# Optimization experiments

Hardware: AMD Instinct MI355X
Metric: run time of the kernel (lower is better)

## Reference

```python
import jax, jax.numpy as jnp
import numpy as np

B, LATENT = 8192, 1024
NR, NC = 12, 12                      # nb_rows, nb_cols
H0, W0 = NR + 2, NC + 2              # 14x14 after reshape
EPS = 1e-5
SLOPE = 0.01                         # LeakyReLU default


def setup_inputs() -> dict:
    key = jax.random.key(0)
    ks = jax.random.split(key, 9)
    s = 0.05
    return {
        "x": jax.random.normal(ks[0], (B, LATENT), jnp.float32),
        "fc_w": jax.random.normal(ks[1], (H0 * W0 * 36, LATENT), jnp.float32) * s,
        "fc_b": jax.random.normal(ks[2], (H0 * W0 * 36,), jnp.float32) * s,
        "conv_w": jax.random.normal(ks[3], (16, 36, 2, 2), jnp.float32) * s,
        "conv_b": jax.random.normal(ks[4], (16,), jnp.float32) * s,
        "gamma": jnp.ones((16,), jnp.float32),
        "beta": jnp.zeros((16,), jnp.float32),
        # locally-connected weights: (out_ch, in_ch, Hout, Wout, k*k)
        "lw1": jax.random.normal(ks[5], (6, 16, H0 - 1, W0 - 1, 4), jnp.float32) * s,
        "lw2": jax.random.normal(ks[6], (1, 6, H0 - 2, W0 - 2, 4), jnp.float32) * s,
    }


def _leaky(x):
    return jnp.where(x >= 0, x, SLOPE * x)


def _local_conv2(x, w):
    # x: (B,C,H,W); w: (O,C,Ho,Wo,4) with k=2, stride 1, no padding
    Ho, Wo = w.shape[2], w.shape[3]
    patches = jnp.stack(
        [x[:, :, dy:dy + Ho, dx:dx + Wo] for dy in (0, 1) for dx in (0, 1)],
        axis=-1)  # (B,C,Ho,Wo,4)
    return jnp.einsum('bchwk,ochwk->bohw', patches, w)


def reference(x, fc_w, fc_b, conv_w, conv_b, gamma, beta, lw1, lw2):
    # fc -> view(B, H0, W0, 36) -> permute to NCHW
    h = x @ fc_w.T + fc_b
    h = h.reshape(B, H0, W0, 36).transpose(0, 3, 1, 2)  # (B,36,14,14)
    # Conv2d k=2 padding='same' (torch pads bottom/right for even kernels)
    h = jax.lax.conv_general_dilated(
        h, conv_w, window_strides=(1, 1), padding=((0, 1), (0, 1)),
        dimension_numbers=('NCHW', 'OIHW', 'NCHW')) + conv_b[None, :, None, None]
    h = _leaky(h)
    # BatchNorm2d (training mode: batch stats, biased var)
    mu = h.mean(axis=(0, 2, 3), keepdims=True)
    var = h.var(axis=(0, 2, 3), keepdims=True)
    h = (h - mu) * jax.lax.rsqrt(var + EPS)
    h = h * gamma[None, :, None, None] + beta[None, :, None, None]
    # locally-connected stack: 14x14 -> 13x13 -> 12x12
    h = _leaky(_local_conv2(h, lw1))
    return _local_conv2(h, lw2)  # (B,1,12,12)
```

## Files before the change

### kernel.cpp

```cpp
#include <hip/hip_runtime.h>


#define SLOPE 0.01f

typedef __bf16 bf16x8 __attribute__((ext_vector_type(8)));
typedef float f32x4 __attribute__((ext_vector_type(4)));

typedef const __attribute__((address_space(1))) void* gas_ptr;
typedef __attribute__((address_space(3))) void* las_ptr;

__device__ __forceinline__ void load16_to_lds(const void* g, void* l) {
  __builtin_amdgcn_global_load_lds((gas_ptr)g, (las_ptr)l, 16, 0, 0);
}

__device__ __forceinline__ unsigned short f2bf(float f) {
  union { float f; unsigned int u; } v; v.f = f;
  unsigned int r = v.u + 0x7FFFu + ((v.u >> 16) & 1u);
  return (unsigned short)(r >> 16);
}
__device__ __forceinline__ float bfbits2f(unsigned int bits16) {
  union { unsigned int u; float f; } v; v.u = bits16 << 16;
  return v.f;
}
__device__ __forceinline__ float leaky(float v) { return v >= 0.f ? v : SLOPE * v; }

__global__ void k_cast_x(const float* __restrict__ x, unsigned short* __restrict__ xb,
                         float* __restrict__ stats_col) {
  if (blockIdx.x == 0)
    for (int i = threadIdx.x; i < 6400; i += 256) stats_col[i] = 0.f;
  int gid = blockIdx.x * 256 + threadIdx.x;
  const float4* x4 = (const float4*)x;
  float4 a = x4[gid * 2], b = x4[gid * 2 + 1];
  union { unsigned short s[8]; uint4 v; } o;
  o.s[0] = f2bf(a.x); o.s[1] = f2bf(a.y); o.s[2] = f2bf(a.z); o.s[3] = f2bf(a.w);
  o.s[4] = f2bf(b.x); o.s[5] = f2bf(b.y); o.s[6] = f2bf(b.z); o.s[7] = f2bf(b.w);
  ((uint4*)xb)[gid] = o.v;
}

__global__ void k_fold(const float* __restrict__ fc_w, const float* __restrict__ fc_b,
                       const float* __restrict__ conv_w, const float* __restrict__ conv_b,
                       unsigned short* __restrict__ Wc, float* __restrict__ bc) {
  int blk = blockIdx.y, kq = blockIdx.x, t = threadIdx.x;
  if (blk == 196) {
    uint4 z = make_uint4(0, 0, 0, 0);
    for (int i = t; i < 64 * 64; i += 256) {
      int r = i >> 6, qq = i & 63;
      *(uint4*)(Wc + (3136 + r) * 1024 + kq * 256 + qq * 8) = z;
    }
    if (kq == 0) for (int i = 3136 + t; i < 3200; i += 256) bc[i] = 0.f;
    return;
  }
  __shared__ float cw[2304];
  for (int i = t; i < 2304; i += 256) cw[i] = conv_w[i];
  __syncthreads();
  int i0 = blk / 14, j0 = blk - (blk / 14) * 14;
  int k = kq * 256 + t;
  float acc[16];
#pragma unroll
  for (int o = 0; o < 16; o++) acc[o] = 0.f;
  for (int c = 0; c < 36; c++) {
#pragma unroll
    for (int dy = 0; dy < 2; dy++) {
      int ii = i0 + dy; if (ii > 13) continue;
#pragma unroll
      for (int dx = 0; dx < 2; dx++) {
        int jj = j0 + dx; if (jj > 13) continue;
        float f = fc_w[((ii * 14 + jj) * 36 + c) * 1024 + k];
        int kk = dy * 2 + dx;
#pragma unroll
        for (int o = 0; o < 16; o++) acc[o] += cw[(o * 36 + c) * 4 + kk] * f;
      }
    }
  }
#pragma unroll
  for (int o = 0; o < 16; o++)
    Wc[(o * 196 + i0 * 14 + j0) * 1024 + k] = f2bf(acc[o]);
  if (kq == 0 && t < 16) {
    int o = t;
    float b = conv_b[o];
    for (int c = 0; c < 36; c++)
      for (int dy = 0; dy < 2; dy++) {
        int ii = i0 + dy; if (ii > 13) continue;
        for (int dx = 0; dx < 2; dx++) {
          int jj = j0 + dx; if (jj > 13) continue;
          b += cw[(o * 36 + c) * 4 + dy * 2 + dx] * fc_b[(ii * 14 + jj) * 36 + c];
        }
      }
    bc[o * 196 + i0 * 14 + j0] = b;
  }
}

__global__ __launch_bounds__(256, 2) void k_gemm(const unsigned short* __restrict__ Xb,
                                                 const unsigned short* __restrict__ Wcb,
                                                 const float* __restrict__ bc,
                                                 unsigned short* __restrict__ h2,
                                                 float* __restrict__ stats_col) {
  __shared__ __align__(16) char lds[16384];
  const int t = threadIdx.x;
  const int w = t >> 6, lane = t & 63;
  const int quad = lane >> 4, l15 = lane & 15;
  const int lid = blockIdx.x;
  const int m0 = (lid & 63) * 128, n0 = (lid >> 6) * 128;
  const int mrow = t & 127, tko = t >> 7;
  const unsigned short* ga = Xb + (m0 + mrow) * 1024 + tko * 8;
  const unsigned short* gb = Wcb + (n0 + mrow) * 1024 + tko * 8;
  char* lA = lds;
  char* lB = lds + 8192;
  const int wbase = w * 1024;
  const int wm0 = (w >> 1) * 64, wn0 = (w & 1) * 64;

  f32x4 acc[4][4];
#pragma unroll
  for (int a = 0; a < 4; a++)
#pragma unroll
    for (int b = 0; b < 4; b++) acc[a][b] = (f32x4){0.f, 0.f, 0.f, 0.f};

  for (int kb = 0; kb < 1024; kb += 32) {
    __syncthreads();
    load16_to_lds(ga + kb,      lA + wbase);
    load16_to_lds(ga + kb + 16, lA + 4096 + wbase);
    load16_to_lds(gb + kb,      lB + wbase);
    load16_to_lds(gb + kb + 16, lB + 4096 + wbase);
    __syncthreads();

    bf16x8 af[4], bfr[4];
#pragma unroll
    for (int mb = 0; mb < 4; mb++)
      af[mb] = *(const bf16x8*)(lA + quad * 2048 + (wm0 + mb * 16 + l15) * 16);
#pragma unroll
    for (int nb = 0; nb < 4; nb++)
      bfr[nb] = *(const bf16x8*)(lB + quad * 2048 + (wn0 + nb * 16 + l15) * 16);
#pragma unroll
    for (int mb = 0; mb < 4; mb++)
#pragma unroll
      for (int nb = 0; nb < 4; nb++)
        acc[mb][nb] = __builtin_amdgcn_mfma_f32_16x16x32_bf16(af[mb], bfr[nb], acc[mb][nb], 0, 0, 0);
  }

#pragma unroll
  for (int nb = 0; nb < 4; nb++) {
    int col = n0 + wn0 + nb * 16 + l15;
    float bias = bc[col];
    float s = 0.f, s2 = 0.f;
    unsigned short* base = h2 + col * 8192 + m0 + wm0 + quad * 4;
#pragma unroll
    for (int mb = 0; mb < 4; mb++) {
      union { unsigned short u[4]; uint2 v; } pk;
#pragma unroll
      for (int r = 0; r < 4; r++) {
        float v = leaky(acc[mb][nb][r] + bias);
        s += v; s2 += v * v;
        pk.u[r] = f2bf(v);
      }
      *(uint2*)(base + mb * 16) = pk.v;
    }
    s  += __shfl_xor(s, 16, 64);  s  += __shfl_xor(s, 32, 64);
    s2 += __shfl_xor(s2, 16, 64); s2 += __shfl_xor(s2, 32, 64);
    if (quad == 0) {
      atomicAdd(&stats_col[col], s);
      atomicAdd(&stats_col[3200 + col], s2);
    }
  }
}

__global__ void k_bnscale(const float* __restrict__ stats_col,
                          const float* __restrict__ gamma, const float* __restrict__ beta,
                          float* __restrict__ scbuf) {
  __shared__ float chs[16], chs2[16];
  int t = threadIdx.x;
  if (t < 16) { chs[t] = 0.f; chs2[t] = 0.f; }
  __syncthreads();
  for (int col = t; col < 3136; col += 256) {
    int o = col / 196;
    atomicAdd(&chs[o], stats_col[col]);
    atomicAdd(&chs2[o], stats_col[3200 + col]);
  }
  __syncthreads();
  if (t < 16) {
    const float inv = 1.f / 1605632.f;
    float mean = chs[t] * inv;
    float var = chs2[t] * inv - mean * mean;
    float sc = gamma[t] * rsqrtf(var + 1e-5f);
    scbuf[t] = sc; scbuf[16 + t] = beta[t] - mean * sc;
  }
}

__global__ __launch_bounds__(64) void k_tail1(const unsigned short* __restrict__ h2,
                                              const float* __restrict__ scbuf,
                                              const float* __restrict__ lw1,
                                              unsigned short* __restrict__ h4) {
  const int m = blockIdx.x * 64 + threadIdx.x;
  const int y = blockIdx.y;
  float acc[6][13];
#pragma unroll
  for (int o = 0; o < 6; o++)
#pragma unroll
    for (int x = 0; x < 13; x++) acc[o][x] = 0.f;

  for (int c = 0; c < 16; c++) {
    float scc = scbuf[c], shc = scbuf[16 + c];
    const unsigned short* p0 = h2 + (c * 196 + y * 14) * 8192 + m;
    float r0[14], r1[14];
#pragma unroll
    for (int x = 0; x < 14; x++) {
      r0[x] = bfbits2f(p0[x * 8192]) * scc + shc;
      r1[x] = bfbits2f(p0[(14 + x) * 8192]) * scc + shc;
    }
#pragma unroll
    for (int o = 0; o < 6; o++) {
      const float* wp = lw1 + (((o * 16 + c) * 13 + y) * 13) * 4;
#pragma unroll
      for (int x = 0; x < 13; x++)
        acc[o][x] += r0[x] * wp[4 * x] + r0[x + 1] * wp[4 * x + 1] +
                     r1[x] * wp[4 * x + 2] + r1[x + 1] * wp[4 * x + 3];
    }
  }
  unsigned short* q = h4 + y * 13 * 8192 + m;
#pragma unroll
  for (int o = 0; o < 6; o++)
#pragma unroll
    for (int x = 0; x < 13; x++)
      q[(o * 169 + x) * 8192] = f2bf(leaky(acc[o][x]));
}

__global__ __launch_bounds__(256) void k_tail2(const unsigned short* __restrict__ h4,
                                               const float* __restrict__ lw2,
                                               float* __restrict__ out) {
  const int lane = threadIdx.x & 63, w = threadIdx.x >> 6;
  const int m = blockIdx.x * 64 + lane;
  const int y = blockIdx.y * 4 + w;
  float acc[12];
#pragma unroll
  for (int x = 0; x < 12; x++) acc[x] = 0.f;
  for (int c = 0; c < 6; c++) {
    const unsigned short* p = h4 + (c * 13 + y) * 13 * 8192 + m;
    float r0[13], r1[13];
#pragma unroll
    for (int x = 0; x < 13; x++) {
      r0[x] = bfbits2f(p[x * 8192]);
      r1[x] = bfbits2f(p[(13 + x) * 8192]);
    }
    const float* wp = lw2 + ((c * 12 + y) * 12) * 4;
#pragma unroll
    for (int x = 0; x < 12; x++)
      acc[x] += r0[x] * wp[4 * x] + r0[x + 1] * wp[4 * x + 1] +
                r1[x] * wp[4 * x + 2] + r1[x + 1] * wp[4 * x + 3];
  }
  float* op = out + m * 144 + y * 12;
#pragma unroll
  for (int x = 0; x < 12; x++) op[x] = acc[x];
}

extern "C" void kernel_launch(void* const* d_in, const int* in_sizes, int n_in,
                              void* d_out, int out_size, void* d_ws, size_t ws_size,
                              hipStream_t stream) {
  const float* x      = (const float*)d_in[0];
  const float* fc_w   = (const float*)d_in[1];
  const float* fc_b   = (const float*)d_in[2];
  const float* conv_w = (const float*)d_in[3];
  const float* conv_b = (const float*)d_in[4];
  const float* gamma  = (const float*)d_in[5];
  const float* beta   = (const float*)d_in[6];
  const float* lw1    = (const float*)d_in[7];
  const float* lw2    = (const float*)d_in[8];

  char* ws = (char*)d_ws;
  unsigned short* Xb        = (unsigned short*)(ws);
  unsigned short* h4T       = (unsigned short*)(ws);
  unsigned short* Wc        = (unsigned short*)(ws + 16777216);
  float*          bc        = (float*)(ws + 23330816);
  float*          stats_col = (float*)(ws + 23343616);
  float*          scbuf     = (float*)(ws + 23369216);
  unsigned short* h2T       = (unsigned short*)(ws + 23369344);

  k_cast_x<<<4096, 256, 0, stream>>>(x, Xb, stats_col);
  k_fold<<<dim3(4, 197), 256, 0, stream>>>(fc_w, fc_b, conv_w, conv_b, Wc, bc);
  k_gemm<<<1600, 256, 0, stream>>>(Xb, Wc, bc, h2T, stats_col);
  k_bnscale<<<1, 256, 0, stream>>>(stats_col, gamma, beta, scbuf);
  k_tail1<<<dim3(128, 13), 64, 0, stream>>>(h2T, scbuf, lw1, h4T);
  k_tail2<<<dim3(128, 3), 256, 0, stream>>>(h4T, lw2, (float*)d_out);
}
```

Measured before the change: 444.3 us.

## Double-buffer GEMM with register prefetch and fuse prep and BN-scale kernels

The GEMM now stages global loads through registers into two LDS buffers. The next K-tile's loads are issued before the MFMAs and the tile is stored to the other buffer afterwards, so each iteration needs one barrier instead of two and memory latency can overlap with compute. Occupancy is raised to three blocks per SM. The x-cast and weight-fold kernels are merged into a single launch, and the BN scale/shift reduction is folded into the first tail kernel, which now uses 256-thread blocks. This removes two launches, but every tail block repeats the small per-channel stat reduction. The prefetch also reads slightly past row ends on the last iterations.

```diff
diff --git a/kernel.cpp b/kernel.cpp
--- a/kernel.cpp
+++ b/kernel.cpp
@@ -5,13 +5,6 @@
 
 typedef __bf16 bf16x8 __attribute__((ext_vector_type(8)));
 typedef float f32x4 __attribute__((ext_vector_type(4)));
-
-typedef const __attribute__((address_space(1))) void* gas_ptr;
-typedef __attribute__((address_space(3))) void* las_ptr;
-
-__device__ __forceinline__ void load16_to_lds(const void* g, void* l) {
-  __builtin_amdgcn_global_load_lds((gas_ptr)g, (las_ptr)l, 16, 0, 0);
-}
 
 __device__ __forceinline__ unsigned short f2bf(float f) {
   union { float f; unsigned int u; } v; v.f = f;
@@ -24,27 +17,30 @@
 }
 __device__ __forceinline__ float leaky(float v) { return v >= 0.f ? v : SLOPE * v; }
 
-__global__ void k_cast_x(const float* __restrict__ x, unsigned short* __restrict__ xb,
-                         float* __restrict__ stats_col) {
-  if (blockIdx.x == 0)
-    for (int i = threadIdx.x; i < 6400; i += 256) stats_col[i] = 0.f;
-  int gid = blockIdx.x * 256 + threadIdx.x;
-  const float4* x4 = (const float4*)x;
-  float4 a = x4[gid * 2], b = x4[gid * 2 + 1];
-  union { unsigned short s[8]; uint4 v; } o;
-  o.s[0] = f2bf(a.x); o.s[1] = f2bf(a.y); o.s[2] = f2bf(a.z); o.s[3] = f2bf(a.w);
-  o.s[4] = f2bf(b.x); o.s[5] = f2bf(b.y); o.s[6] = f2bf(b.z); o.s[7] = f2bf(b.w);
-  ((uint4*)xb)[gid] = o.v;
-}
-
-__global__ void k_fold(const float* __restrict__ fc_w, const float* __restrict__ fc_b,
+__global__ void k_prep(const float* __restrict__ x, unsigned short* __restrict__ xb,
+                       float* __restrict__ stats_col,
+                       const float* __restrict__ fc_w, const float* __restrict__ fc_b,
                        const float* __restrict__ conv_w, const float* __restrict__ conv_b,
                        unsigned short* __restrict__ Wc, float* __restrict__ bc) {
-  int blk = blockIdx.y, kq = blockIdx.x, t = threadIdx.x;
+  const int t = threadIdx.x;
+  if (blockIdx.x < 4096) {
+    if (blockIdx.x == 0)
+      for (int i = t; i < 6400; i += 256) stats_col[i] = 0.f;
+    int gid = blockIdx.x * 256 + t;
+    const float4* x4 = (const float4*)x;
+    float4 a = x4[gid * 2], b = x4[gid * 2 + 1];
+    union { unsigned short s[8]; uint4 v; } o;
+    o.s[0] = f2bf(a.x); o.s[1] = f2bf(a.y); o.s[2] = f2bf(a.z); o.s[3] = f2bf(a.w);
+    o.s[4] = f2bf(b.x); o.s[5] = f2bf(b.y); o.s[6] = f2bf(b.z); o.s[7] = f2bf(b.w);
+    ((uint4*)xb)[gid] = o.v;
+    return;
+  }
+  int bid = blockIdx.x - 4096;
+  int kq = bid & 3, blk = bid >> 2;
   if (blk == 196) {
     uint4 z = make_uint4(0, 0, 0, 0);
-    for (int i = t; i < 64 * 64; i += 256) {
-      int r = i >> 6, qq = i & 63;
+    for (int i = t; i < 64 * 32; i += 256) {
+      int r = i >> 5, qq = i & 31;
       *(uint4*)(Wc + (3136 + r) * 1024 + kq * 256 + qq * 8) = z;
     }
     if (kq == 0) for (int i = 3136 + t; i < 3200; i += 256) bc[i] = 0.f;
@@ -90,12 +86,12 @@
   }
 }
 
-__global__ __launch_bounds__(256, 2) void k_gemm(const unsigned short* __restrict__ Xb,
+__global__ __launch_bounds__(256, 3) void k_gemm(const unsigned short* __restrict__ Xb,
                                                  const unsigned short* __restrict__ Wcb,
                                                  const float* __restrict__ bc,
                                                  unsigned short* __restrict__ h2,
                                                  float* __restrict__ stats_col) {
-  __shared__ __align__(16) char lds[16384];
+  __shared__ __align__(16) char lds[32768];
   const int t = threadIdx.x;
   const int w = t >> 6, lane = t & 63;
   const int quad = lane >> 4, l15 = lane & 15;
@@ -104,9 +100,7 @@
   const int mrow = t & 127, tko = t >> 7;
   const unsigned short* ga = Xb + (m0 + mrow) * 1024 + tko * 8;
   const unsigned short* gb = Wcb + (n0 + mrow) * 1024 + tko * 8;
-  char* lA = lds;
-  char* lB = lds + 8192;
-  const int wbase = w * 1024;
+  char* const wA = lds + tko * 2048 + mrow * 16;
   const int wm0 = (w >> 1) * 64, wn0 = (w & 1) * 64;
 
   f32x4 acc[4][4];
@@ -115,26 +109,42 @@
 #pragma unroll
     for (int b = 0; b < 4; b++) acc[a][b] = (f32x4){0.f, 0.f, 0.f, 0.f};
 
-  for (int kb = 0; kb < 1024; kb += 32) {
-    __syncthreads();
-    load16_to_lds(ga + kb,      lA + wbase);
-    load16_to_lds(ga + kb + 16, lA + 4096 + wbase);
-    load16_to_lds(gb + kb,      lB + wbase);
-    load16_to_lds(gb + kb + 16, lB + 4096 + wbase);
-    __syncthreads();
-
+  uint4 ra[2][2], rb[2][2];
+  ra[0][0] = *(const uint4*)(ga);      ra[0][1] = *(const uint4*)(ga + 16);
+  rb[0][0] = *(const uint4*)(gb);      rb[0][1] = *(const uint4*)(gb + 16);
+  *(uint4*)(wA)        = ra[0][0];  *(uint4*)(wA + 4096)        = ra[0][1];
+  *(uint4*)(wA + 8192) = rb[0][0];  *(uint4*)(wA + 8192 + 4096) = rb[0][1];
+  ra[1][0] = *(const uint4*)(ga + 32); ra[1][1] = *(const uint4*)(ga + 48);
+  rb[1][0] = *(const uint4*)(gb + 32); rb[1][1] = *(const uint4*)(gb + 48);
+  __syncthreads();
+
+#pragma unroll 2
+  for (int j = 0; j < 32; j++) {
+    const int cur = j & 1, nxt = cur ^ 1;
+    const char* rbuf = lds + cur * 16384;
     bf16x8 af[4], bfr[4];
 #pragma unroll
     for (int mb = 0; mb < 4; mb++)
-      af[mb] = *(const bf16x8*)(lA + quad * 2048 + (wm0 + mb * 16 + l15) * 16);
+      af[mb] = *(const bf16x8*)(rbuf + quad * 2048 + (wm0 + mb * 16 + l15) * 16);
 #pragma unroll
     for (int nb = 0; nb < 4; nb++)
-      bfr[nb] = *(const bf16x8*)(lB + quad * 2048 + (wn0 + nb * 16 + l15) * 16);
+      bfr[nb] = *(const bf16x8*)(rbuf + 8192 + quad * 2048 + (wn0 + nb * 16 + l15) * 16);
+    {
+      const int off = (j + 2) * 32;
+      ra[cur][0] = *(const uint4*)(ga + off);      ra[cur][1] = *(const uint4*)(ga + off + 16);
+      rb[cur][0] = *(const uint4*)(gb + off);      rb[cur][1] = *(const uint4*)(gb + off + 16);
+    }
 #pragma unroll
     for (int mb = 0; mb < 4; mb++)
 #pragma unroll
       for (int nb = 0; nb < 4; nb++)
         acc[mb][nb] = __builtin_amdgcn_mfma_f32_16x16x32_bf16(af[mb], bfr[nb], acc[mb][nb], 0, 0, 0);
+    {
+      char* wb_ = lds + nxt * 16384 + tko * 2048 + mrow * 16;
+      *(uint4*)(wb_)        = ra[nxt][0];  *(uint4*)(wb_ + 4096)        = ra[nxt][1];
+      *(uint4*)(wb_ + 8192) = rb[nxt][0];  *(uint4*)(wb_ + 8192 + 4096) = rb[nxt][1];
+    }
+    __syncthreads();
   }
 
 #pragma unroll
@@ -163,33 +173,33 @@
   }
 }
 
-__global__ void k_bnscale(const float* __restrict__ stats_col,
-                          const float* __restrict__ gamma, const float* __restrict__ beta,
-                          float* __restrict__ scbuf) {
-  __shared__ float chs[16], chs2[16];
-  int t = threadIdx.x;
-  if (t < 16) { chs[t] = 0.f; chs2[t] = 0.f; }
+__global__ __launch_bounds__(256) void k_tail1(const unsigned short* __restrict__ h2,
+                                               const float* __restrict__ stats_col,
+                                               const float* __restrict__ gamma,
+                                               const float* __restrict__ beta,
+                                               const float* __restrict__ lw1,
+                                               unsigned short* __restrict__ h4) {
+  __shared__ float chs[32];
+  __shared__ float sc_s[16], sh_s[16];
+  const int t = threadIdx.x;
+  if (t < 32) chs[t] = 0.f;
   __syncthreads();
   for (int col = t; col < 3136; col += 256) {
     int o = col / 196;
     atomicAdd(&chs[o], stats_col[col]);
-    atomicAdd(&chs2[o], stats_col[3200 + col]);
+    atomicAdd(&chs[16 + o], stats_col[3200 + col]);
   }
   __syncthreads();
   if (t < 16) {
     const float inv = 1.f / 1605632.f;
     float mean = chs[t] * inv;
-    float var = chs2[t] * inv - mean * mean;
+    float var = chs[16 + t] * inv - mean * mean;
     float sc = gamma[t] * rsqrtf(var + 1e-5f);
-    scbuf[t] = sc; scbuf[16 + t] = beta[t] - mean * sc;
-  }
-}
-
-__global__ __launch_bounds__(64) void k_tail1(const unsigned short* __restrict__ h2,
-                                              const float* __restrict__ scbuf,
-                                              const float* __restrict__ lw1,
-                                              unsigned short* __restrict__ h4) {
-  const int m = blockIdx.x * 64 + threadIdx.x;
+    sc_s[t] = sc; sh_s[t] = beta[t] - mean * sc;
+  }
+  __syncthreads();
+
+  const int m = blockIdx.x * 256 + t;
   const int y = blockIdx.y;
   float acc[6][13];
 #pragma unroll
@@ -198,7 +208,7 @@
     for (int x = 0; x < 13; x++) acc[o][x] = 0.f;
 
   for (int c = 0; c < 16; c++) {
-    float scc = scbuf[c], shc = scbuf[16 + c];
+    float scc = sc_s[c], shc = sh_s[c];
     const unsigned short* p0 = h2 + (c * 196 + y * 14) * 8192 + m;
     float r0[14], r1[14];
 #pragma unroll
@@ -270,13 +280,10 @@
   unsigned short* Wc        = (unsigned short*)(ws + 16777216);
   float*          bc        = (float*)(ws + 23330816);
   float*          stats_col = (float*)(ws + 23343616);
-  float*          scbuf     = (float*)(ws + 23369216);
   unsigned short* h2T       = (unsigned short*)(ws + 23369344);
 
-  k_cast_x<<<4096, 256, 0, stream>>>(x, Xb, stats_col);
-  k_fold<<<dim3(4, 197), 256, 0, stream>>>(fc_w, fc_b, conv_w, conv_b, Wc, bc);
+  k_prep<<<4884, 256, 0, stream>>>(x, Xb, stats_col, fc_w, fc_b, conv_w, conv_b, Wc, bc);
   k_gemm<<<1600, 256, 0, stream>>>(Xb, Wc, bc, h2T, stats_col);
-  k_bnscale<<<1, 256, 0, stream>>>(stats_col, gamma, beta, scbuf);
-  k_tail1<<<dim3(128, 13), 64, 0, stream>>>(h2T, scbuf, lw1, h4T);
+  k_tail1<<<dim3(32, 13), 256, 0, stream>>>(h2T, stats_col, gamma, beta, lw1, h4T);
   k_tail2<<<dim3(128, 3), 256, 0, stream>>>(h4T, lw2, (float*)d_out);
 }
```

New measurement: 672.5 us. +51.4%, slower.
